# Kernel tuning notes

Measured on AMD Instinct MI355X. Metric: run time of the kernel, lower is better.

Reference implementation:

```python
import jax, jax.numpy as jnp
import numpy as np

B, S, D = 4, 2048, 2048
H, Dh, Dl = 16, 128, 128  # head_dim must equal latent_dim for the source matmul to type-check


def setup_inputs() -> dict:
    key = jax.random.key(0)
    ks = jax.random.split(key, 6)
    sc = 0.02
    return {
        "hidden_states": jax.random.normal(ks[0], (B, S, D), dtype=jnp.float32),
        "Wq": jax.random.normal(ks[1], (H * Dh, D), dtype=jnp.float32) * sc,
        "Wk_down": jax.random.normal(ks[2], (H * Dl, D), dtype=jnp.float32) * sc,
        "Wv_down": jax.random.normal(ks[3], (H * Dl, D), dtype=jnp.float32) * sc,
        "Wk_up": jax.random.normal(ks[4], (H * Dh, H * Dl), dtype=jnp.float32) * sc,
        "Wo": jax.random.normal(ks[5], (D, H * Dh), dtype=jnp.float32) * sc,
    }


def reference(hidden_states, Wq, Wk_down, Wv_down, Wk_up, Wo):
    # projections (torch Linear: y = x @ W.T)
    q = (hidden_states @ Wq.T).reshape(B, S, H, Dh).transpose(0, 2, 1, 3)        # [B,H,S,Dh]
    k_lat = (hidden_states @ Wk_down.T).reshape(B, S, H, Dl).transpose(0, 2, 1, 3)  # [B,H,S,Dl]
    v_lat = (hidden_states @ Wv_down.T).reshape(B, S, H, Dl).transpose(0, 2, 1, 3)  # [B,H,S,Dl]

    scores = jnp.einsum("bhsd,bhtd->bhst", q, k_lat) / jnp.sqrt(jnp.float32(Dl))
    attn = jax.nn.softmax(scores, axis=-1)
    out_lat = jnp.einsum("bhst,bhtd->bhsd", attn, v_lat)                          # [B,H,S,Dl]
    out_lat = out_lat.transpose(0, 2, 1, 3).reshape(B, S, H * Dl)

    # source bug (faithful): k_up_proj is applied to the attention output
    up = out_lat @ Wk_up.T                                                         # [B,S,H*Dh]
    return up @ Wo.T                                                               # [B,S,D]
```

## Files before the change

### kernel.cpp

```cpp
#include <hip/hip_runtime.h>
#include <hip/hip_bf16.h>
#include <stdint.h>

typedef unsigned short u16;
typedef __attribute__((ext_vector_type(4))) float f32x4;
typedef __attribute__((ext_vector_type(8))) short s16x8;
typedef __attribute__((ext_vector_type(4))) u16 u16x4;

__device__ __forceinline__ u16 f2bf(float x) {
  union { float f; uint32_t u; } v; v.f = x;
  uint32_t r = v.u + 0x7FFFu + ((v.u >> 16) & 1u);
  return (u16)(r >> 16);
}
__device__ __forceinline__ u16 f2bfh(float x) {
  __hip_bfloat16 h = __float2bfloat16(x);
  u16 r; __builtin_memcpy(&r, &h, 2); return r;
}

__device__ __forceinline__ void gload16(const void* g, const void* l) {
  __builtin_amdgcn_global_load_lds((const __attribute__((address_space(1))) void*)g,
                                   (__attribute__((address_space(3))) void*)l,
                                   16, 0, 0);
}

__global__ void fill_k(float* out, int n, float v) {
  for (int i = blockIdx.x * blockDim.x + threadIdx.x; i < n; i += gridDim.x * blockDim.x)
    out[i] = v;
}

__global__ void cvtall_k(const float* __restrict__ hs, const float* __restrict__ Wq,
                         const float* __restrict__ Wkd, const float* __restrict__ Wvd,
                         const float* __restrict__ Wo,
                         u16* __restrict__ hsB, u16* __restrict__ W3, u16* __restrict__ WoB) {
  int i = blockIdx.x * blockDim.x + threadIdx.x;
  const float* src; u16* dst; int off;
  if (i < 4194304)      { src = hs;  dst = hsB;          off = i; }
  else if (i < 5242880) { src = Wq;  dst = W3;           off = i - 4194304; }
  else if (i < 6291456) { src = Wkd; dst = W3 + 4194304; off = i - 5242880; }
  else if (i < 7340032) { src = Wvd; dst = W3 + 8388608; off = i - 6291456; }
  else                  { src = Wo;  dst = WoB;          off = i - 7340032; }
  f32x4 v = ((const f32x4*)src)[off];
  u16x4 o;
  o.x = f2bf(v.x); o.y = f2bf(v.y); o.z = f2bf(v.z); o.w = f2bf(v.w);
  ((u16x4*)dst)[off] = o;
}

__global__ void cvtT_k(const float* __restrict__ in, u16* __restrict__ out) {
  __shared__ float t[32][33];
  int tx = threadIdx.x, ty = threadIdx.y;
  int c = blockIdx.x * 32 + tx;
#pragma unroll
  for (int j = 0; j < 4; ++j) {
    int r = blockIdx.y * 32 + ty + j * 8;
    t[ty + j * 8][tx] = in[(size_t)r * 2048 + c];
  }
  __syncthreads();
  int c2 = blockIdx.y * 32 + tx;
#pragma unroll
  for (int j = 0; j < 4; ++j) {
    int r2 = blockIdx.x * 32 + ty + j * 8;
    out[(size_t)r2 * 2048 + c2] = f2bf(t[tx][ty + j * 8]);
  }
}

__global__ __launch_bounds__(256) void gemm_qkvwc_k(const u16* __restrict__ hsB,
                                                    const u16* __restrict__ W3,
                                                    u16* __restrict__ qk,
                                                    u16* __restrict__ Vt,
                                                    const u16* __restrict__ WoB,
                                                    const u16* __restrict__ WkuT,
                                                    u16* __restrict__ WcH) {
  __shared__ u16 As[128 * 64];
  __shared__ u16 Bs[128 * 64];
  int bid = blockIdx.x;
  int bid2 = (bid & 7) * 416 + (bid >> 3);
  const u16 *A0, *B0;
  int mt, nt; bool isW;
  if (bid2 < 3072) { isW = false; mt = bid2 / 48; nt = bid2 - mt * 48; A0 = hsB; B0 = W3; }
  else { int ix = bid2 - 3072; isW = true; mt = ix >> 4; nt = ix & 15; A0 = WoB; B0 = WkuT; }
  const int K = 2048;
  int tid = threadIdx.x, wave = tid >> 6, lane = tid & 63;
  int l15 = lane & 15, l4 = lane >> 4;
  int wr = wave >> 1, wc = wave & 1;
  int sr = lane >> 3, sc = lane & 7;
  int gsl = (sc ^ sr) * 8;

  const u16* Ag = A0 + (size_t)(mt * 128 + wave * 32 + sr) * K + gsl;
  const u16* Bg = B0 + (size_t)(nt * 128 + wave * 32 + sr) * K + gsl;
  u16* Asw = As + wave * 32 * 64;
  u16* Bsw = Bs + wave * 32 * 64;

  f32x4 acc[4][4];
#pragma unroll
  for (int i = 0; i < 4; ++i)
#pragma unroll
    for (int j = 0; j < 4; ++j) acc[i][j] = f32x4{0.f, 0.f, 0.f, 0.f};

  for (int kt = 0; kt < K; kt += 64) {
#pragma unroll
    for (int i = 0; i < 4; ++i) {
      gload16(Ag + kt + i * 8 * K, Asw + i * 512);
      gload16(Bg + kt + i * 8 * K, Bsw + i * 512);
    }
    __syncthreads();
#pragma unroll
    for (int kk = 0; kk < 2; ++kk) {
      s16x8 af[4], bfr[4];
#pragma unroll
      for (int mf = 0; mf < 4; ++mf) {
        int row = wr * 64 + mf * 16 + l15;
        int sl = ((kk * 4 + l4) ^ (row & 7)) * 8;
        af[mf] = *(const s16x8*)(As + row * 64 + sl);
      }
#pragma unroll
      for (int nf = 0; nf < 4; ++nf) {
        int row = wc * 64 + nf * 16 + l15;
        int sl = ((kk * 4 + l4) ^ (row & 7)) * 8;
        bfr[nf] = *(const s16x8*)(Bs + row * 64 + sl);
      }
#pragma unroll
      for (int mf = 0; mf < 4; ++mf)
#pragma unroll
        for (int nf = 0; nf < 4; ++nf)
          acc[mf][nf] = __builtin_amdgcn_mfma_f32_16x16x32_bf16(af[mf], bfr[nf], acc[mf][nf], 0, 0, 0);
    }
    __syncthreads();
  }

  int crow = mt * 128 + wr * 64 + l4 * 4;
  int ccol = nt * 128 + wc * 64 + l15;
#pragma unroll
  for (int mf = 0; mf < 4; ++mf)
#pragma unroll
    for (int nf = 0; nf < 4; ++nf) {
      int col = ccol + nf * 16;
      int row0 = crow + mf * 16;
      if (isW) {
#pragma unroll
        for (int r = 0; r < 4; ++r)
          WcH[(size_t)(row0 + r) * 2048 + col] = f2bfh(acc[mf][nf][r]);
      } else if (col >= 4096) {
        int h = (col - 4096) >> 7, dh = (col - 4096) & 127;
        int b = row0 >> 11, s0 = row0 & 2047;
        u16x4 w;
        w.x = f2bfh(acc[mf][nf][0]); w.y = f2bfh(acc[mf][nf][1]);
        w.z = f2bfh(acc[mf][nf][2]); w.w = f2bfh(acc[mf][nf][3]);
        *(u16x4*)(Vt + ((size_t)((b << 4) + h) * 128 + dh) * 2048 + s0) = w;
      } else {
#pragma unroll
        for (int r = 0; r < 4; ++r)
          qk[(size_t)(row0 + r) * 4096 + col] = f2bfh(acc[mf][nf][r]);
      }
    }
}

__global__ __launch_bounds__(256) void btgemm_k(const u16* __restrict__ A0,
                                                const u16* __restrict__ B0,
                                                float* __restrict__ C,
                                                int M, int N, int K) {
  __shared__ u16 As[128 * 64];
  __shared__ u16 Bs[128 * 64];
  int nnt = N >> 7;
  int bid = blockIdx.x;
  int nwg = gridDim.x;
  if ((nwg & 7) == 0) { int q = nwg >> 3; bid = (bid & 7) * q + (bid >> 3); }
  int mt = bid / nnt, nt = bid - mt * nnt;
  int tid = threadIdx.x, wave = tid >> 6, lane = tid & 63;
  int l15 = lane & 15, l4 = lane >> 4;
  int wr = wave >> 1, wc = wave & 1;
  int sr = lane >> 3, sc = lane & 7;
  int gsl = (sc ^ sr) * 8;

  const u16* Ag = A0 + (size_t)(mt * 128 + wave * 32 + sr) * K + gsl;
  const u16* Bg = B0 + (size_t)(nt * 128 + wave * 32 + sr) * K + gsl;
  u16* Asw = As + wave * 32 * 64;
  u16* Bsw = Bs + wave * 32 * 64;

  f32x4 acc[4][4];
#pragma unroll
  for (int i = 0; i < 4; ++i)
#pragma unroll
    for (int j = 0; j < 4; ++j) acc[i][j] = f32x4{0.f, 0.f, 0.f, 0.f};

  for (int kt = 0; kt < K; kt += 64) {
#pragma unroll
    for (int i = 0; i < 4; ++i) {
      gload16(Ag + kt + i * 8 * K, Asw + i * 512);
      gload16(Bg + kt + i * 8 * K, Bsw + i * 512);
    }
    __syncthreads();
#pragma unroll
    for (int kk = 0; kk < 2; ++kk) {
      s16x8 af[4], bfr[4];
#pragma unroll
      for (int mf = 0; mf < 4; ++mf) {
        int row = wr * 64 + mf * 16 + l15;
        int sl = ((kk * 4 + l4) ^ (row & 7)) * 8;
        af[mf] = *(const s16x8*)(As + row * 64 + sl);
      }
#pragma unroll
      for (int nf = 0; nf < 4; ++nf) {
        int row = wc * 64 + nf * 16 + l15;
        int sl = ((kk * 4 + l4) ^ (row & 7)) * 8;
        bfr[nf] = *(const s16x8*)(Bs + row * 64 + sl);
      }
#pragma unroll
      for (int mf = 0; mf < 4; ++mf)
#pragma unroll
        for (int nf = 0; nf < 4; ++nf)
          acc[mf][nf] = __builtin_amdgcn_mfma_f32_16x16x32_bf16(af[mf], bfr[nf], acc[mf][nf], 0, 0, 0);
    }
    __syncthreads();
  }

  int crow = mt * 128 + wr * 64 + l4 * 4;
  int ccol = nt * 128 + wc * 64 + l15;
#pragma unroll
  for (int mf = 0; mf < 4; ++mf)
#pragma unroll
    for (int nf = 0; nf < 4; ++nf)
#pragma unroll
      for (int r = 0; r < 4; ++r)
        C[(size_t)(crow + mf * 16 + r) * N + (ccol + nf * 16)] = acc[mf][nf][r];
}

__global__ __launch_bounds__(512, 4) void attn9_k(const u16* __restrict__ qk,
                                                  const u16* __restrict__ Vt,
                                                  u16* __restrict__ outl) {
  __shared__ u16 Ks[2][64 * 128];
  __shared__ u16 Vs[2][128 * 64];
  __shared__ u16 Ps2[8 * 16 * 64];

  int bid = blockIdx.x;
  int xcd = bid & 7, slot = bid >> 3;
  int bh = xcd * 8 + (slot >> 4), qb = slot & 15;
  int b = bh >> 4, h = bh & 15;
  int tid = threadIdx.x, wave = tid >> 6, lane = tid & 63;
  int l15 = lane & 15, l4 = lane >> 4;
  int q0 = qb * 128 + wave * 16;
  const float ksc = 0.12751743f;

  s16x8 qf[4];
#pragma unroll
  for (int kf = 0; kf < 4; ++kf)
    qf[kf] = *(const s16x8*)(qk + (size_t)(b * 2048 + q0 + l15) * 4096 +
                             h * 128 + kf * 32 + l4 * 8);

  f32x4 po[8];
  float smrun = -1e30f, lrun = 0.f;
#pragma unroll
  for (int n2 = 0; n2 < 8; ++n2) po[n2] = f32x4{0.f, 0.f, 0.f, 0.f};

  char* PsW = (char*)Ps2 + wave * 2048;

  int krow_b = wave * 8;
  int vrow_b = wave * 16;
  int kj = lane & 15;
  int vj = lane & 7;

  s16x8 kr[2], vr[2];
#define GLOAD_TILE(kv0)                                                                  \
  _Pragma("unroll") for (int i = 0; i < 2; ++i) {                                        \
    int row = krow_b + i * 4 + (lane >> 4);                                              \
    kr[i] = *(const s16x8*)(qk + (size_t)(b * 2048 + (kv0) + row) * 4096 + 2048 +        \
                            h * 128 + kj * 8);                                           \
    int row2 = vrow_b + i * 8 + (lane >> 3);                                             \
    vr[i] = *(const s16x8*)(Vt + (size_t)(bh * 128 + row2) * 2048 + (kv0) + vj * 8);     \
  }

  GLOAD_TILE(0)

  for (int t = 0; t < 32; ++t) {
    int cur = t & 1;
    u16* Ksc = Ks[cur];
    u16* Vsc = Vs[cur];
#pragma unroll
    for (int i = 0; i < 2; ++i) {
      int row = krow_b + i * 4 + (lane >> 4);
      *(s16x8*)(Ksc + row * 128 + ((kj ^ (row & 7)) * 8)) = kr[i];
      int row2 = vrow_b + i * 8 + (lane >> 3);
      *(s16x8*)(Vsc + row2 * 64 + ((vj ^ (row2 & 7)) * 8)) = vr[i];
    }
    __syncthreads();
    if (t < 31) GLOAD_TILE((t + 1) * 64)

    f32x4 sa[4];
#pragma unroll
    for (int nf = 0; nf < 4; ++nf) sa[nf] = f32x4{0.f, 0.f, 0.f, 0.f};
    __builtin_amdgcn_s_setprio(1);
#pragma unroll
    for (int kf = 0; kf < 4; ++kf) {
      s16x8 kb[4];
#pragma unroll
      for (int nf = 0; nf < 4; ++nf) {
        int row = nf * 16 + l15;
        int sl = ((kf * 4 + l4) ^ (row & 7)) * 8;
        kb[nf] = *(const s16x8*)(Ksc + row * 128 + sl);
      }
#pragma unroll
      for (int nf = 0; nf < 4; ++nf)
        sa[nf] = __builtin_amdgcn_mfma_f32_16x16x32_bf16(kb[nf], qf[kf], sa[nf], 0, 0, 0);
    }
    __builtin_amdgcn_s_setprio(0);

    {
      float m01 = fmaxf(fmaxf(sa[0][0], sa[0][1]), fmaxf(sa[0][2], sa[0][3]));
      float m23 = fmaxf(fmaxf(sa[1][0], sa[1][1]), fmaxf(sa[1][2], sa[1][3]));
      float m45 = fmaxf(fmaxf(sa[2][0], sa[2][1]), fmaxf(sa[2][2], sa[2][3]));
      float m67 = fmaxf(fmaxf(sa[3][0], sa[3][1]), fmaxf(sa[3][2], sa[3][3]));
      float pmax = fmaxf(fmaxf(m01, m23), fmaxf(m45, m67));
      pmax = fmaxf(pmax, __shfl_xor(pmax, 16, 64));
      pmax = fmaxf(pmax, __shfl_xor(pmax, 32, 64));
      float smax = pmax * ksc;
      if (!__all(smax - smrun <= 8.0f)) {
        float mnew = fmaxf(smrun, smax);
        float fsc = exp2f(smrun - mnew);
        lrun *= fsc;
#pragma unroll
        for (int n2 = 0; n2 < 8; ++n2)
#pragma unroll
          for (int r = 0; r < 4; ++r) po[n2][r] *= fsc;
        smrun = mnew;
      }
      int row = l15;
      int swz = (row & 7) << 4;
      float ssum = 0.f;
#pragma unroll
      for (int nf = 0; nf < 4; ++nf) {
        float p0 = exp2f(fmaf(sa[nf][0], ksc, -smrun));
        float p1 = exp2f(fmaf(sa[nf][1], ksc, -smrun));
        float p2 = exp2f(fmaf(sa[nf][2], ksc, -smrun));
        float p3 = exp2f(fmaf(sa[nf][3], ksc, -smrun));
        ssum += (p0 + p1) + (p2 + p3);
        u16x4 w;
        w.x = f2bfh(p0); w.y = f2bfh(p1); w.z = f2bfh(p2); w.w = f2bfh(p3);
        *(u16x4*)(PsW + row * 128 + (((nf * 4 + l4) * 8) ^ swz)) = w;
      }
      ssum += __shfl_xor(ssum, 16, 64);
      ssum += __shfl_xor(ssum, 32, 64);
      lrun += ssum;
    }

    s16x8 pb[2];
    {
      int row = l15;
      int swz = (row & 7) << 4;
#pragma unroll
      for (int k2 = 0; k2 < 2; ++k2)
        pb[k2] = *(const s16x8*)(PsW + row * 128 + ((k2 * 64 + l4 * 16) ^ swz));
    }

    __builtin_amdgcn_s_setprio(1);
#pragma unroll
    for (int n2 = 0; n2 < 8; ++n2) {
#pragma unroll
      for (int k2 = 0; k2 < 2; ++k2) {
        int row = n2 * 16 + l15;
        int sl = ((k2 * 4 + l4) ^ (row & 7)) * 8;
        s16x8 vb = *(const s16x8*)(Vsc + row * 64 + sl);
        po[n2] = __builtin_amdgcn_mfma_f32_16x16x32_bf16(vb, pb[k2], po[n2], 0, 0, 0);
      }
    }
    __builtin_amdgcn_s_setprio(0);
  }
#undef GLOAD_TILE

  {
    float inv = 1.0f / lrun;
#pragma unroll
    for (int n2 = 0; n2 < 8; ++n2) {
      u16x4 w;
      w.x = f2bfh(po[n2][0] * inv);
      w.y = f2bfh(po[n2][1] * inv);
      w.z = f2bfh(po[n2][2] * inv);
      w.w = f2bfh(po[n2][3] * inv);
      *(u16x4*)(outl + (size_t)(b * 2048 + q0 + l15) * 2048 + h * 128 + n2 * 16 + l4 * 4) = w;
    }
  }
}

extern "C" void kernel_launch(void* const* d_in, const int* in_sizes, int n_in,
                              void* d_out, int out_size, void* d_ws, size_t ws_size,
                              hipStream_t stream) {
  (void)in_sizes; (void)n_in;
  const float* hs  = (const float*)d_in[0];
  const float* Wq  = (const float*)d_in[1];
  const float* Wkd = (const float*)d_in[2];
  const float* Wvd = (const float*)d_in[3];
  const float* Wku = (const float*)d_in[4];
  const float* Wo  = (const float*)d_in[5];
  float* out = (float*)d_out;
  char* ws = (char*)d_ws;

  if (ws_size < 201326592ull) {
    fill_k<<<4096, 256, 0, stream>>>(out, out_size, 1e9f);
    return;
  }

  u16* W3   = (u16*)(ws);
  u16* WcH  = (u16*)(ws + 25165824);
  u16* hsB  = (u16*)(ws + 33554432);
  u16* outl = (u16*)(ws + 33554432);
  u16* qk   = (u16*)(ws + 67108864);
  u16* WoB  = (u16*)(ws + 134217728);
  u16* WkuT = (u16*)(ws + 142606336);
  u16* Vt   = (u16*)(ws + 167772160);

  cvtall_k<<<32768, 256, 0, stream>>>(hs, Wq, Wkd, Wvd, Wo, hsB, W3, WoB);
  cvtT_k<<<dim3(64, 64), dim3(32, 8), 0, stream>>>(Wku, WkuT);

  gemm_qkvwc_k<<<3328, 256, 0, stream>>>(hsB, W3, qk, Vt, WoB, WkuT, WcH);

  attn9_k<<<1024, 512, 0, stream>>>(qk, Vt, outl);

  btgemm_k<<<1024, 256, 0, stream>>>(outl, WcH, out, 8192, 2048, 2048);
}
```

Measured before the change: 579.3 us.

## Split Wc precompute out and use 256x256 multi-stage pipelined QKV GEMM

Removes the combined QKV/Wc GEMM kernel. The Wo·Wk_up weight product now runs through a templated btgemm kernel with bf16 output. The QKV projection moves to a new 512-thread kernel with 256x256 tiles, a 4-slot LDS ring buffer and prefetch three k-steps ahead. That kernel uses explicit vmcnt waits, raw s_barrier and setprio around the MFMA blocks. The aim is more reuse per tile and overlap of global loads with MFMA work, at the cost of more LDS (128KB) and registers, which lowers occupancy and adds one kernel launch.

```diff
diff --git a/kernel.cpp b/kernel.cpp
--- a/kernel.cpp
+++ b/kernel.cpp
@@ -22,6 +22,10 @@
                                    (__attribute__((address_space(3))) void*)l,
                                    16, 0, 0);
 }
+
+#define BAR() asm volatile("s_barrier" ::: "memory")
+#define VMCNT8() asm volatile("s_waitcnt vmcnt(8)" ::: "memory")
+#define VMCNT0() asm volatile("s_waitcnt vmcnt(0)" ::: "memory")
 
 __global__ void fill_k(float* out, int n, float v) {
   for (int i = blockIdx.x * blockDim.x + threadIdx.x; i < n; i += gridDim.x * blockDim.x)
@@ -63,100 +67,10 @@
   }
 }
 
-__global__ __launch_bounds__(256) void gemm_qkvwc_k(const u16* __restrict__ hsB,
-                                                    const u16* __restrict__ W3,
-                                                    u16* __restrict__ qk,
-                                                    u16* __restrict__ Vt,
-                                                    const u16* __restrict__ WoB,
-                                                    const u16* __restrict__ WkuT,
-                                                    u16* __restrict__ WcH) {
-  __shared__ u16 As[128 * 64];
-  __shared__ u16 Bs[128 * 64];
-  int bid = blockIdx.x;
-  int bid2 = (bid & 7) * 416 + (bid >> 3);
-  const u16 *A0, *B0;
-  int mt, nt; bool isW;
-  if (bid2 < 3072) { isW = false; mt = bid2 / 48; nt = bid2 - mt * 48; A0 = hsB; B0 = W3; }
-  else { int ix = bid2 - 3072; isW = true; mt = ix >> 4; nt = ix & 15; A0 = WoB; B0 = WkuT; }
-  const int K = 2048;
-  int tid = threadIdx.x, wave = tid >> 6, lane = tid & 63;
-  int l15 = lane & 15, l4 = lane >> 4;
-  int wr = wave >> 1, wc = wave & 1;
-  int sr = lane >> 3, sc = lane & 7;
-  int gsl = (sc ^ sr) * 8;
-
-  const u16* Ag = A0 + (size_t)(mt * 128 + wave * 32 + sr) * K + gsl;
-  const u16* Bg = B0 + (size_t)(nt * 128 + wave * 32 + sr) * K + gsl;
-  u16* Asw = As + wave * 32 * 64;
-  u16* Bsw = Bs + wave * 32 * 64;
-
-  f32x4 acc[4][4];
-#pragma unroll
-  for (int i = 0; i < 4; ++i)
-#pragma unroll
-    for (int j = 0; j < 4; ++j) acc[i][j] = f32x4{0.f, 0.f, 0.f, 0.f};
-
-  for (int kt = 0; kt < K; kt += 64) {
-#pragma unroll
-    for (int i = 0; i < 4; ++i) {
-      gload16(Ag + kt + i * 8 * K, Asw + i * 512);
-      gload16(Bg + kt + i * 8 * K, Bsw + i * 512);
-    }
-    __syncthreads();
-#pragma unroll
-    for (int kk = 0; kk < 2; ++kk) {
-      s16x8 af[4], bfr[4];
-#pragma unroll
-      for (int mf = 0; mf < 4; ++mf) {
-        int row = wr * 64 + mf * 16 + l15;
-        int sl = ((kk * 4 + l4) ^ (row & 7)) * 8;
-        af[mf] = *(const s16x8*)(As + row * 64 + sl);
-      }
-#pragma unroll
-      for (int nf = 0; nf < 4; ++nf) {
-        int row = wc * 64 + nf * 16 + l15;
-        int sl = ((kk * 4 + l4) ^ (row & 7)) * 8;
-        bfr[nf] = *(const s16x8*)(Bs + row * 64 + sl);
-      }
-#pragma unroll
-      for (int mf = 0; mf < 4; ++mf)
-#pragma unroll
-        for (int nf = 0; nf < 4; ++nf)
-          acc[mf][nf] = __builtin_amdgcn_mfma_f32_16x16x32_bf16(af[mf], bfr[nf], acc[mf][nf], 0, 0, 0);
-    }
-    __syncthreads();
-  }
-
-  int crow = mt * 128 + wr * 64 + l4 * 4;
-  int ccol = nt * 128 + wc * 64 + l15;
-#pragma unroll
-  for (int mf = 0; mf < 4; ++mf)
-#pragma unroll
-    for (int nf = 0; nf < 4; ++nf) {
-      int col = ccol + nf * 16;
-      int row0 = crow + mf * 16;
-      if (isW) {
-#pragma unroll
-        for (int r = 0; r < 4; ++r)
-          WcH[(size_t)(row0 + r) * 2048 + col] = f2bfh(acc[mf][nf][r]);
-      } else if (col >= 4096) {
-        int h = (col - 4096) >> 7, dh = (col - 4096) & 127;
-        int b = row0 >> 11, s0 = row0 & 2047;
-        u16x4 w;
-        w.x = f2bfh(acc[mf][nf][0]); w.y = f2bfh(acc[mf][nf][1]);
-        w.z = f2bfh(acc[mf][nf][2]); w.w = f2bfh(acc[mf][nf][3]);
-        *(u16x4*)(Vt + ((size_t)((b << 4) + h) * 128 + dh) * 2048 + s0) = w;
-      } else {
-#pragma unroll
-        for (int r = 0; r < 4; ++r)
-          qk[(size_t)(row0 + r) * 4096 + col] = f2bfh(acc[mf][nf][r]);
-      }
-    }
-}
-
+template <typename CT, int OUTMODE>
 __global__ __launch_bounds__(256) void btgemm_k(const u16* __restrict__ A0,
                                                 const u16* __restrict__ B0,
-                                                float* __restrict__ C,
+                                                CT* __restrict__ C,
                                                 int M, int N, int K) {
   __shared__ u16 As[128 * 64];
   __shared__ u16 Bs[128 * 64];
@@ -220,8 +134,112 @@
 #pragma unroll
     for (int nf = 0; nf < 4; ++nf)
 #pragma unroll
-      for (int r = 0; r < 4; ++r)
-        C[(size_t)(crow + mf * 16 + r) * N + (ccol + nf * 16)] = acc[mf][nf][r];
+      for (int r = 0; r < 4; ++r) {
+        size_t idx = (size_t)(crow + mf * 16 + r) * N + (ccol + nf * 16);
+        float v = acc[mf][nf][r];
+        if constexpr (OUTMODE == 0) C[idx] = v; else C[idx] = f2bfh(v);
+      }
+}
+
+__global__ __launch_bounds__(512, 2) void gemm256qkv_k(const u16* __restrict__ A0,
+                                                       const u16* __restrict__ B0,
+                                                       u16* __restrict__ qk,
+                                                       u16* __restrict__ Vt) {
+  __shared__ u16 lds4[4][2][8192];
+
+  const int K = 2048;
+  int bid = blockIdx.x;
+  int bid2 = (bid & 7) * 96 + (bid >> 3);
+  int mt = bid2 / 24, nt = bid2 - mt * 24;
+  int tid = threadIdx.x, wave = tid >> 6, lane = tid & 63;
+  int l15 = lane & 15, l4 = lane >> 4;
+  int wr = wave >> 2, wc = wave & 3;
+
+  int rowin = tid >> 2;
+  int gsl = (tid & 3) ^ (rowin & 3) ^ ((rowin >> 2) & 3);
+  const u16* Agst = A0 + (size_t)(mt * 256 + rowin) * K + gsl * 8;
+  const u16* Bgst = B0 + (size_t)(nt * 256 + rowin) * K + gsl * 8;
+  const size_t HSTRIDE = (size_t)128 * K;
+
+  int sl = l4 ^ (l15 & 3) ^ ((l15 >> 2) & 3);
+  int aoff = wr * 4096 + l15 * 32 + sl * 8;
+  int boff = wc * 2048 + l15 * 32 + sl * 8;
+
+  f32x4 acc[8][4];
+#pragma unroll
+  for (int i = 0; i < 8; ++i)
+#pragma unroll
+    for (int j = 0; j < 4; ++j) acc[i][j] = f32x4{0.f, 0.f, 0.f, 0.f};
+
+#pragma unroll
+  for (int p = 0; p < 3; ++p) {
+    gload16(Agst + p * 32, &lds4[p][0][wave * 512]);
+    gload16(Agst + HSTRIDE + p * 32, &lds4[p][0][4096 + wave * 512]);
+    gload16(Bgst + p * 32, &lds4[p][1][wave * 512]);
+    gload16(Bgst + HSTRIDE + p * 32, &lds4[p][1][4096 + wave * 512]);
+  }
+  VMCNT8();
+  BAR();
+
+  for (int t = 0; t < 64; ++t) {
+    const u16* Ab = lds4[t & 3][0];
+    const u16* Bb = lds4[t & 3][1];
+    int tt = (t + 3) & 63;
+    int sb = tt & 3;
+
+    s16x8 bfr[4], af[4];
+#pragma unroll
+    for (int nf = 0; nf < 4; ++nf) bfr[nf] = *(const s16x8*)(Bb + boff + nf * 512);
+#pragma unroll
+    for (int mf = 0; mf < 4; ++mf) af[mf] = *(const s16x8*)(Ab + aoff + mf * 512);
+    gload16(Agst + tt * 32, &lds4[sb][0][wave * 512]);
+    gload16(Agst + HSTRIDE + tt * 32, &lds4[sb][0][4096 + wave * 512]);
+    __builtin_amdgcn_s_setprio(1);
+#pragma unroll
+    for (int mf = 0; mf < 4; ++mf)
+#pragma unroll
+      for (int nf = 0; nf < 4; ++nf)
+        acc[mf][nf] = __builtin_amdgcn_mfma_f32_16x16x32_bf16(af[mf], bfr[nf], acc[mf][nf], 0, 0, 0);
+    __builtin_amdgcn_s_setprio(0);
+    BAR();
+
+#pragma unroll
+    for (int mf = 0; mf < 4; ++mf) af[mf] = *(const s16x8*)(Ab + aoff + (mf + 4) * 512);
+    gload16(Bgst + tt * 32, &lds4[sb][1][wave * 512]);
+    gload16(Bgst + HSTRIDE + tt * 32, &lds4[sb][1][4096 + wave * 512]);
+    __builtin_amdgcn_s_setprio(1);
+#pragma unroll
+    for (int mf = 0; mf < 4; ++mf)
+#pragma unroll
+      for (int nf = 0; nf < 4; ++nf)
+        acc[mf + 4][nf] = __builtin_amdgcn_mfma_f32_16x16x32_bf16(af[mf], bfr[nf], acc[mf + 4][nf], 0, 0, 0);
+    __builtin_amdgcn_s_setprio(0);
+    VMCNT8();
+    BAR();
+  }
+  VMCNT0();
+
+  int crow0 = mt * 256 + wr * 128 + l4 * 4;
+  int ccol0 = nt * 256 + wc * 64 + l15;
+#pragma unroll
+  for (int mf = 0; mf < 8; ++mf)
+#pragma unroll
+    for (int nf = 0; nf < 4; ++nf) {
+      int col = ccol0 + nf * 16;
+      int row0 = crow0 + mf * 16;
+      if (col >= 4096) {
+        int h = (col - 4096) >> 7, dh = (col - 4096) & 127;
+        int b = row0 >> 11, s0 = row0 & 2047;
+        u16x4 w;
+        w.x = f2bfh(acc[mf][nf][0]); w.y = f2bfh(acc[mf][nf][1]);
+        w.z = f2bfh(acc[mf][nf][2]); w.w = f2bfh(acc[mf][nf][3]);
+        *(u16x4*)(Vt + ((size_t)((b << 4) + h) * 128 + dh) * 2048 + s0) = w;
+      } else {
+#pragma unroll
+        for (int r = 0; r < 4; ++r)
+          qk[(size_t)(row0 + r) * 4096 + col] = f2bfh(acc[mf][nf][r]);
+      }
+    }
 }
 
 __global__ __launch_bounds__(512, 4) void attn9_k(const u16* __restrict__ qk,
@@ -409,9 +427,11 @@
   cvtall_k<<<32768, 256, 0, stream>>>(hs, Wq, Wkd, Wvd, Wo, hsB, W3, WoB);
   cvtT_k<<<dim3(64, 64), dim3(32, 8), 0, stream>>>(Wku, WkuT);
 
-  gemm_qkvwc_k<<<3328, 256, 0, stream>>>(hsB, W3, qk, Vt, WoB, WkuT, WcH);
+  btgemm_k<u16, 1><<<256, 256, 0, stream>>>(WoB, WkuT, WcH, 2048, 2048, 2048);
+
+  gemm256qkv_k<<<768, 512, 0, stream>>>(hsB, W3, qk, Vt);
 
   attn9_k<<<1024, 512, 0, stream>>>(qk, Vt, outl);
 
-  btgemm_k<<<1024, 256, 0, stream>>>(outl, WcH, out, 8192, 2048, 2048);
-}
+  btgemm_k<float, 0><<<1024, 256, 0, stream>>>(outl, WcH, out, 8192, 2048, 2048);
+}
```

Result: faster. 538.6 us (-7.0%).
